# Kernel tuning notes

Measured on AMD Instinct MI355X. Metric: run time of the kernel, lower is better.

Reference implementation:

```python
import jax, jax.numpy as jnp
import numpy as np

EPS_NORM = 1e-12   # torch F.normalize eps
EPS_BN = 1e-5      # BatchNorm1d eps
NEG_SLOPE = 0.01   # LeakyReLU default


def _l2_normalize(x, axis):
    # torch F.normalize: x / max(||x||, eps)
    n = jnp.sqrt(jnp.sum(x * x, axis=axis, keepdims=True))
    return x / jnp.maximum(n, EPS_NORM)


def setup_inputs() -> dict:
    key = jax.random.key(0)
    k1, k2, k3, k4, k5, k6, k7 = jax.random.split(key, 7)
    B, C, N, M, OUT = 8, 128, 4096, 4096, 128
    return {
        "input": jax.random.normal(k1, (B, C, N), dtype=jnp.float32),
        "target_g": jax.random.normal(k2, (B, C, M), dtype=jnp.float32),
        "weight": jax.random.normal(k3, (C, OUT), dtype=jnp.float32) * (1.0 / np.sqrt(OUT)),
        "gamma": jax.random.normal(k4, (OUT,), dtype=jnp.float32),
        "beta": jax.random.normal(k5, (OUT,), dtype=jnp.float32),
        "running_mean": jax.random.normal(k6, (OUT,), dtype=jnp.float32),
        "running_var": jax.random.uniform(k7, (OUT,), dtype=jnp.float32, minval=0.5, maxval=1.5),
    }


def reference(input, target_g, weight, gamma, beta, running_mean, running_var):
    # input: [B, C, N], target_g: [B, C, M]
    # cosine-similarity adjacency: [B, M, N]
    tg = _l2_normalize(target_g, axis=1)
    inp_n = _l2_normalize(input, axis=1)
    adj = jnp.einsum('bcm,bcn->bmn', tg, inp_n)
    adj = jax.nn.softmax(adj, axis=-1)
    # aggregate: [B, M, C]
    agg = jnp.einsum('bmn,bcn->bmc', adj, input)
    # project: [B, M, OUT] -> permute to [B, OUT, M]
    out = jnp.einsum('bmc,co->bom', agg, weight)
    # LeakyReLU then BatchNorm1d (eval mode, running stats)
    out = jnp.where(out >= 0, out, NEG_SLOPE * out)
    inv = jax.lax.rsqrt(running_var + EPS_BN)
    out = (out - running_mean[None, :, None]) * (inv * gamma)[None, :, None] + beta[None, :, None]
    return out
```

## Files before the change

### kernel.cpp

```cpp
#include <hip/hip_runtime.h>
#include <hip/hip_bf16.h>

#define BATCH 8
#define CDIM 128
#define NDIM 4096

typedef __bf16 bf16x8 __attribute__((ext_vector_type(8)));
typedef float f32x4 __attribute__((ext_vector_type(4)));
typedef float f32x16 __attribute__((ext_vector_type(16)));
typedef unsigned u32x4 __attribute__((ext_vector_type(4)));

#define QT_OFF 0u
#define KT_OFF 8388608u
#define VB_OFF 16777216u
#define WT_OFF 25165824u
#define SC_OFF (WT_OFF + 32768u)
#define BI_OFF (SC_OFF + 512u)

__device__ __forceinline__ f32x4 mfma16(bf16x8 a, bf16x8 b, f32x4 c) {
    return __builtin_amdgcn_mfma_f32_16x16x32_bf16(a, b, c, 0, 0, 0);
}
__device__ __forceinline__ f32x16 mfma32(bf16x8 a, bf16x8 b, f32x16 c) {
    return __builtin_amdgcn_mfma_f32_32x32x16_bf16(a, b, c, 0, 0, 0);
}

__device__ __forceinline__ unsigned pack2bf(float a, float b) {
    unsigned short ul = __builtin_bit_cast(unsigned short, (__bf16)a);
    unsigned short uh = __builtin_bit_cast(unsigned short, (__bf16)b);
    return (unsigned)ul | ((unsigned)uh << 16);
}

__device__ __forceinline__ void glds16(const void* g, void* l) {
    __builtin_amdgcn_global_load_lds((__attribute__((address_space(1))) void*)(void*)g,
                                     (__attribute__((address_space(3))) void*)l, 16, 0, 0);
}

__device__ __forceinline__ void pls32(unsigned& a, unsigned& b) {
    asm("v_permlane32_swap_b32 %0, %1" : "+v"(a), "+v"(b));
}

__global__ __launch_bounds__(256) void prep_nt(const float* __restrict__ input,
                                               const float* __restrict__ tg,
                                               const float* __restrict__ wgt,
                                               const float* __restrict__ gamma,
                                               const float* __restrict__ beta,
                                               const float* __restrict__ mean,
                                               const float* __restrict__ var,
                                               void* __restrict__ ws) {
    __shared__ float Tt[64][129];
    __shared__ float psum[4][64];
    __shared__ float rn[64];
    const int n0 = blockIdx.x * 64;
    const int b  = blockIdx.y;
    const int tid = threadIdx.x;
    const float* src = (blockIdx.z == 0 ? input : tg) + (size_t)b * CDIM * NDIM;

    #pragma unroll
    for (int i = 0; i < 8; ++i) {
        int f = tid + i * 256;
        int c = f >> 4, j4 = f & 15;
        float4 v = *(const float4*)(src + (size_t)c * NDIM + n0 + j4 * 4);
        Tt[j4 * 4 + 0][c] = v.x;
        Tt[j4 * 4 + 1][c] = v.y;
        Tt[j4 * 4 + 2][c] = v.z;
        Tt[j4 * 4 + 3][c] = v.w;
    }
    __syncthreads();
    {
        int j = tid & 63, part = tid >> 6;
        float ss = 0.f;
        #pragma unroll 8
        for (int c = part * 32; c < part * 32 + 32; ++c) { float x = Tt[j][c]; ss += x * x; }
        psum[part][j] = ss;
    }
    __syncthreads();
    if (tid < 64) {
        float s = psum[0][tid] + psum[1][tid] + psum[2][tid] + psum[3][tid];
        rn[tid] = 1.0f / fmaxf(sqrtf(s), 1e-12f);
    }
    __syncthreads();

    __hip_bfloat16* dstT = (__hip_bfloat16*)((char*)ws + (blockIdx.z == 0 ? KT_OFF : QT_OFF))
                           + ((size_t)b * NDIM + n0) * CDIM;
    #pragma unroll
    for (int i = 0; i < 8; ++i) {
        int f = tid + i * 256;
        int j = f >> 5, c4 = f & 31;
        float r = rn[j];
        float4 v = *(const float4*)&Tt[j][c4 * 4];
        uint2 pk; pk.x = pack2bf(v.x * r, v.y * r); pk.y = pack2bf(v.z * r, v.w * r);
        *(uint2*)((unsigned short*)dstT + (size_t)j * CDIM + c4 * 4) = pk;
    }
    if (blockIdx.z == 0) {
        __hip_bfloat16* vb = (__hip_bfloat16*)((char*)ws + VB_OFF) + (size_t)b * CDIM * NDIM + n0;
        #pragma unroll
        for (int i = 0; i < 8; ++i) {
            int f = tid + i * 256;
            int c = f >> 4, j4 = f & 15;
            float x0 = Tt[j4 * 4 + 0][c], x1 = Tt[j4 * 4 + 1][c];
            float x2 = Tt[j4 * 4 + 2][c], x3 = Tt[j4 * 4 + 3][c];
            uint2 pv; pv.x = pack2bf(x0, x1); pv.y = pack2bf(x2, x3);
            *(uint2*)((unsigned short*)vb + (size_t)c * NDIM + j4 * 4) = pv;
        }
    } else if (blockIdx.x == 0 && b == 0) {
        __hip_bfloat16* wT = (__hip_bfloat16*)((char*)ws + WT_OFF);
        float* sc = (float*)((char*)ws + SC_OFF);
        float* bi = (float*)((char*)ws + BI_OFF);
        #pragma unroll
        for (int i = 0; i < 64; ++i) {
            int f = tid + i * 256;
            int c = f >> 7, o = f & 127;
            wT[o * 128 + c] = __hip_bfloat16(wgt[c * 128 + o]);
        }
        if (tid < 128) {
            float inv = rsqrtf(var[tid] + 1e-5f);
            float s = inv * gamma[tid];
            sc[tid] = s;
            bi[tid] = beta[tid] - mean[tid] * s;
        }
    }
}

__global__ __launch_bounds__(512, 2) void flash9b(const void* __restrict__ ws_,
                                                  float* __restrict__ out) {
    extern __shared__ char smem[];
    const char* ws = (const char*)ws_;
    const __hip_bfloat16* Qt = (const __hip_bfloat16*)(ws + QT_OFF);
    const __hip_bfloat16* Kt = (const __hip_bfloat16*)(ws + KT_OFF);
    const __hip_bfloat16* Vb = (const __hip_bfloat16*)(ws + VB_OFF);
    const __hip_bfloat16* wT = (const __hip_bfloat16*)(ws + WT_OFF);
    const float* scale = (const float*)(ws + SC_OFF);
    const float* bias  = (const float*)(ws + BI_OFF);

    const int bx = blockIdx.x;
    const int b  = bx & 7;
    const int m0 = (bx >> 3) * 128;
    const int tid = threadIdx.x;
    const int w = tid >> 6, lane = tid & 63;
    const int hf = lane >> 5;
    const int l31 = lane & 31;
    const int nt = w & 1;
    const int mt = w >> 1;

    const char* kgb = (const char*)(Kt + (size_t)b * NDIM * CDIM);
    const char* vgb = (const char*)(Vb + (size_t)b * CDIM * NDIM);

    bf16x8 qb[8];
    {
        const char* qrow = (const char*)Qt + ((size_t)b * NDIM + m0 + mt * 32 + l31) * 256 + hf * 16;
        #pragma unroll
        for (int s = 0; s < 8; ++s) qb[s] = *(const bf16x8*)(qrow + s * 32);
    }

    unsigned kOff[8];
    {
        int nn = nt * 64 + l31;
        #pragma unroll
        for (int s = 0; s < 8; ++s)
            kOff[s] = nn * 256 + (((2 * s + hf) ^ (nn & 15)) * 16);
    }
    unsigned vOff[2][4];
    #pragma unroll
    for (int t = 0; t < 2; ++t)
        #pragma unroll
        for (int ca = 0; ca < 4; ++ca) {
            int c = ca * 32 + l31;
            vOff[t][ca] = 32768 + c * 256 + (((nt * 8 + t * 2 + hf) ^ (c & 15)) * 16);
        }

    const char* kSrc[4]; const char* vSrc[4];
    unsigned kDst[4], vDst[4];
    #pragma unroll
    for (int i = 0; i < 4; ++i) {
        int slot = i * 512 + tid;
        int r = slot >> 4, j = slot & 15;
        kSrc[i] = kgb + r * 256 + ((j ^ (r & 15)) * 16);
        kDst[i] = i * 8192 + w * 1024;
        vSrc[i] = vgb + (size_t)r * 8192 + ((j ^ (r & 15)) * 16);
        vDst[i] = 32768 + i * 8192 + w * 1024;
    }

    f32x16 oacc[4];
    #pragma unroll
    for (int ca = 0; ca < 4; ++ca)
        #pragma unroll
        for (int i = 0; i < 16; ++i) oacc[ca][i] = 0.f;
    float lacc = 0.f;

    #pragma unroll
    for (int i = 0; i < 4; ++i) { glds16(kSrc[i], smem + kDst[i]); kSrc[i] += 32768; }
    #pragma unroll
    for (int i = 0; i < 4; ++i) { glds16(vSrc[i], smem + vDst[i]); vSrc[i] += 256; }

    auto softmax_pf = [&](const f32x16& s, bf16x8* pf) {
        unsigned d[8];
        float lsum = 0.f;
        #pragma unroll
        for (int rq = 0; rq < 4; ++rq) {
            float e0 = __expf(s[rq * 4 + 0] - 1.0f);
            float e1 = __expf(s[rq * 4 + 1] - 1.0f);
            float e2 = __expf(s[rq * 4 + 2] - 1.0f);
            float e3 = __expf(s[rq * 4 + 3] - 1.0f);
            lsum += (e0 + e1) + (e2 + e3);
            d[rq * 2 + 0] = pack2bf(e0, e1);
            d[rq * 2 + 1] = pack2bf(e2, e3);
        }
        lacc += lsum;
        #pragma unroll
        for (int t = 0; t < 2; ++t) {
            pls32(d[4 * t + 0], d[4 * t + 2]);
            pls32(d[4 * t + 1], d[4 * t + 3]);
            u32x4 tv;
            tv.x = d[4 * t + 0]; tv.y = d[4 * t + 1];
            tv.z = d[4 * t + 2]; tv.w = d[4 * t + 3];
            pf[t] = __builtin_bit_cast(bf16x8, tv);
        }
    };

    auto body = [&](const unsigned bo, const bool do_pref) {
        asm volatile("s_waitcnt vmcnt(0) lgkmcnt(0)\ns_barrier" ::: "memory");
        if (do_pref) {
            const unsigned obo = bo ^ 65536u;
            #pragma unroll
            for (int i = 0; i < 4; ++i) { glds16(kSrc[i], smem + (obo + kDst[i])); kSrc[i] += 32768; }
            #pragma unroll
            for (int i = 0; i < 4; ++i) { glds16(vSrc[i], smem + (obo + vDst[i])); vSrc[i] += 256; }
        }
        const char* base = smem + bo;

        bf16x8 kf[16];
        #pragma unroll
        for (int s = 0; s < 8; ++s) kf[s] = *(const bf16x8*)(base + kOff[s]);
        #pragma unroll
        for (int s = 0; s < 8; ++s) kf[8 + s] = *(const bf16x8*)(base + kOff[s] + 8192);

        f32x16 st0, st1;
        #pragma unroll
        for (int i = 0; i < 16; ++i) { st0[i] = 0.f; st1[i] = 0.f; }
        #pragma unroll
        for (int s = 0; s < 8; ++s) st0 = mfma32(kf[s], qb[s], st0);
        #pragma unroll
        for (int s = 0; s < 8; ++s) st1 = mfma32(kf[8 + s], qb[s], st1);

        bf16x8 vf0[8];
        #pragma unroll
        for (int t = 0; t < 2; ++t)
            #pragma unroll
            for (int ca = 0; ca < 4; ++ca)
                vf0[t * 4 + ca] = *(const bf16x8*)(base + vOff[t][ca]);

        bf16x8 pf0[2];
        softmax_pf(st0, pf0);

        #pragma unroll
        for (int t = 0; t < 2; ++t)
            #pragma unroll
            for (int ca = 0; ca < 4; ++ca)
                oacc[ca] = mfma32(vf0[t * 4 + ca], pf0[t], oacc[ca]);

        bf16x8 vf1[8];
        #pragma unroll
        for (int t = 0; t < 2; ++t)
            #pragma unroll
            for (int ca = 0; ca < 4; ++ca)
                vf1[t * 4 + ca] = *(const bf16x8*)(base + (vOff[t][ca] ^ 64u));

        bf16x8 pf1[2];
        softmax_pf(st1, pf1);

        #pragma unroll
        for (int t = 0; t < 2; ++t)
            #pragma unroll
            for (int ca = 0; ca < 4; ++ca)
                oacc[ca] = mfma32(vf1[t * 4 + ca], pf1[t], oacc[ca]);
    };

    for (int ii = 0; ii < 16; ++ii) {
        body(0u, true);
        body(65536u, ii != 15);
    }

    float lw = lacc + __shfl_xor(lacc, 32, 64);
    __syncthreads();
    float* lLds = (float*)(smem + 65536);
    if (lane < 32) lLds[w * 32 + lane] = lw;
    if (w & 1) {
        float4* dst = (float4*)smem + (w >> 1) * 1024 + lane;
        #pragma unroll
        for (int ca = 0; ca < 4; ++ca)
            #pragma unroll
            for (int rq = 0; rq < 4; ++rq) {
                float4 t = { oacc[ca][rq * 4 + 0], oacc[ca][rq * 4 + 1],
                             oacc[ca][rq * 4 + 2], oacc[ca][rq * 4 + 3] };
                dst[(ca * 4 + rq) * 64] = t;
            }
    }
    __syncthreads();
    char* sAgg = smem + 67584;
    if (!(w & 1)) {
        float linv = 1.0f / (lLds[w * 32 + l31] + lLds[(w + 1) * 32 + l31]);
        const float4* srcp = (const float4*)smem + (w >> 1) * 1024 + lane;
        int m = (w >> 1) * 32 + l31;
        char* aggRow = sAgg + m * 256;
        const int mx = (m & 7) << 1;
        #pragma unroll
        for (int ca = 0; ca < 4; ++ca)
            #pragma unroll
            for (int rq = 0; rq < 4; ++rq) {
                float4 ov = srcp[(ca * 4 + rq) * 64];
                float v0 = (oacc[ca][rq * 4 + 0] + ov.x) * linv;
                float v1 = (oacc[ca][rq * 4 + 1] + ov.y) * linv;
                float v2 = (oacc[ca][rq * 4 + 2] + ov.z) * linv;
                float v3 = (oacc[ca][rq * 4 + 3] + ov.w) * linv;
                int cq = ca * 8 + rq * 2 + hf;
                uint2 pk; pk.x = pack2bf(v0, v1); pk.y = pack2bf(v2, v3);
                *(uint2*)(aggRow + ((cq ^ mx) * 8)) = pk;
            }
    }
    __syncthreads();

    const int li = lane & 15, q = lane >> 4;
    const int pm = w * 16 + li;
    f32x4 racc[8];
    #pragma unroll
    for (int ob = 0; ob < 8; ++ob) { racc[ob][0]=0.f; racc[ob][1]=0.f; racc[ob][2]=0.f; racc[ob][3]=0.f; }
    #pragma unroll
    for (int ks = 0; ks < 4; ++ks) {
        int slot8 = ((ks * 4 + q) * 2) ^ ((li & 7) << 1);
        bf16x8 af = *(const bf16x8*)(sAgg + pm * 256 + slot8 * 8);
        #pragma unroll
        for (int ob = 0; ob < 8; ++ob) {
            bf16x8 wf = *(const bf16x8*)((const char*)wT + (ob * 16 + li) * 256 + ks * 64 + q * 16);
            racc[ob] = mfma16(af, wf, racc[ob]);
        }
    }

    float* sRes = (float*)smem;
    #pragma unroll
    for (int ob = 0; ob < 8; ++ob) {
        int oo = ob * 16 + li;
        float sc = scale[oo], bi = bias[oo];
        #pragma unroll
        for (int r = 0; r < 4; ++r) {
            float v = racc[ob][r];
            v = (v >= 0.0f) ? v : 0.01f * v;
            v = v * sc + bi;
            sRes[oo * 132 + w * 16 + q * 4 + r] = v;
        }
    }
    __syncthreads();

    float* outb = out + (size_t)b * CDIM * NDIM + m0;
    #pragma unroll
    for (int i = 0; i < 8; ++i) {
        int f = tid + i * 512;
        int o = f >> 5, mq = f & 31;
        *(float4*)(outb + (size_t)o * NDIM + mq * 4) = *(const float4*)(sRes + o * 132 + mq * 4);
    }
}

extern "C" void kernel_launch(void* const* d_in, const int* in_sizes, int n_in,
                              void* d_out, int out_size, void* d_ws, size_t ws_size,
                              hipStream_t stream) {
    const float* input  = (const float*)d_in[0];
    const float* tg     = (const float*)d_in[1];
    const float* weight = (const float*)d_in[2];
    const float* gamma  = (const float*)d_in[3];
    const float* beta   = (const float*)d_in[4];
    const float* rmean  = (const float*)d_in[5];
    const float* rvar   = (const float*)d_in[6];
    float* out = (float*)d_out;

    (void)in_sizes; (void)n_in; (void)out_size; (void)ws_size;

    hipFuncSetAttribute(reinterpret_cast<const void*>(flash9b),
                        hipFuncAttributeMaxDynamicSharedMemorySize, 131072);

    dim3 gprep(NDIM / 64, BATCH, 2);
    prep_nt<<<gprep, 256, 0, stream>>>(input, tg, weight, gamma, beta, rmean, rvar, d_ws);
    flash9b<<<dim3(256), 512, 131072, stream>>>(d_ws, out);
}
```

Baseline: 181.3 us.

## Defer second-half PV MFMA to next iteration to overlap with barrier and staging

Software-pipelines the attention loop by carrying the second half's softmax probabilities and V fragments in registers, then issuing their PV MFMAs at the start of the next body, after the barrier and prefetch issue. The aim is to fill the wait after the barrier with matrix work and overlap the softmax exp with MFMA execution. In exchange it keeps about ten more bf16x8 vectors live across iterations, which raises register pressure under a 512x2 launch bound and could cause spills.

Result: slower. 221.3 us (+22.1%).

```diff
diff --git a/kernel.cpp b/kernel.cpp
--- a/kernel.cpp
+++ b/kernel.cpp
@@ -121,7 +121,7 @@
     }
 }
 
-__global__ __launch_bounds__(512, 2) void flash9b(const void* __restrict__ ws_,
+__global__ __launch_bounds__(512, 2) void flash10(const void* __restrict__ ws_,
                                                   float* __restrict__ out) {
     extern __shared__ char smem[];
     const char* ws = (const char*)ws_;
@@ -217,15 +217,28 @@
         }
     };
 
-    auto body = [&](const unsigned bo, const bool do_pref) {
+    auto stage = [&](const unsigned obo) {
+        #pragma unroll
+        for (int i = 0; i < 4; ++i) { glds16(kSrc[i], smem + (obo + kDst[i])); kSrc[i] += 32768; }
+        #pragma unroll
+        for (int i = 0; i < 4; ++i) { glds16(vSrc[i], smem + (obo + vDst[i])); vSrc[i] += 256; }
+    };
+
+    auto pv8 = [&](const bf16x8* vf, const bf16x8* pf) {
+        #pragma unroll
+        for (int t = 0; t < 2; ++t)
+            #pragma unroll
+            for (int ca = 0; ca < 4; ++ca)
+                oacc[ca] = mfma32(vf[t * 4 + ca], pf[t], oacc[ca]);
+    };
+
+    bf16x8 pf1c[2];
+    bf16x8 vf1c[8];
+
+    auto body = [&](const unsigned bo, const bool do_pref, const bool do_prev) {
         asm volatile("s_waitcnt vmcnt(0) lgkmcnt(0)\ns_barrier" ::: "memory");
-        if (do_pref) {
-            const unsigned obo = bo ^ 65536u;
-            #pragma unroll
-            for (int i = 0; i < 4; ++i) { glds16(kSrc[i], smem + (obo + kDst[i])); kSrc[i] += 32768; }
-            #pragma unroll
-            for (int i = 0; i < 4; ++i) { glds16(vSrc[i], smem + (obo + vDst[i])); vSrc[i] += 256; }
-        }
+        if (do_pref) stage(bo ^ 65536u);
+        if (do_prev) pv8(vf1c, pf1c);
         const char* base = smem + bo;
 
         bf16x8 kf[16];
@@ -252,33 +265,24 @@
         bf16x8 pf0[2];
         softmax_pf(st0, pf0);
 
+        pv8(vf0, pf0);
+
         #pragma unroll
         for (int t = 0; t < 2; ++t)
             #pragma unroll
             for (int ca = 0; ca < 4; ++ca)
-                oacc[ca] = mfma32(vf0[t * 4 + ca], pf0[t], oacc[ca]);
-
-        bf16x8 vf1[8];
-        #pragma unroll
-        for (int t = 0; t < 2; ++t)
-            #pragma unroll
-            for (int ca = 0; ca < 4; ++ca)
-                vf1[t * 4 + ca] = *(const bf16x8*)(base + (vOff[t][ca] ^ 64u));
-
-        bf16x8 pf1[2];
-        softmax_pf(st1, pf1);
-
-        #pragma unroll
-        for (int t = 0; t < 2; ++t)
-            #pragma unroll
-            for (int ca = 0; ca < 4; ++ca)
-                oacc[ca] = mfma32(vf1[t * 4 + ca], pf1[t], oacc[ca]);
+                vf1c[t * 4 + ca] = *(const bf16x8*)(base + (vOff[t][ca] ^ 64u));
+
+        softmax_pf(st1, pf1c);
     };
 
-    for (int ii = 0; ii < 16; ++ii) {
-        body(0u, true);
-        body(65536u, ii != 15);
-    }
+    body(0u, true, false);
+    body(65536u, true, true);
+    for (int ii = 1; ii < 16; ++ii) {
+        body(0u, true, true);
+        body(65536u, ii != 15, true);
+    }
+    pv8(vf1c, pf1c);
 
     float lw = lacc + __shfl_xor(lacc, 32, 64);
     __syncthreads();
@@ -373,10 +377,10 @@
 
     (void)in_sizes; (void)n_in; (void)out_size; (void)ws_size;
 
-    hipFuncSetAttribute(reinterpret_cast<const void*>(flash9b),
+    hipFuncSetAttribute(reinterpret_cast<const void*>(flash10),
                         hipFuncAttributeMaxDynamicSharedMemorySize, 131072);
 
     dim3 gprep(NDIM / 64, BATCH, 2);
     prep_nt<<<gprep, 256, 0, stream>>>(input, tg, weight, gamma, beta, rmean, rvar, d_ws);
-    flash9b<<<dim3(256), 512, 131072, stream>>>(d_ws, out);
-}
+    flash10<<<dim3(256), 512, 131072, stream>>>(d_ws, out);
+}
```
